# Kernel optimization log

Measured on AMD Instinct MI355X. Metric: run time of the kernel, lower is better.

Reference implementation:

```python
import jax, jax.numpy as jnp
import numpy as np

B, F, V, E, T, NTOK, G, D = 8192, 64, 1000, 64, 2, 16, 4, 256
LN_EPS = 1e-5


def setup_inputs() -> dict:
    key = jax.random.key(0)
    ks = jax.random.split(key, 5)
    int_feats = jax.random.randint(ks[0], (B, F), 0, V, dtype=jnp.int64)
    missing_mask = jax.random.randint(ks[1], (B, F), 0, 2, dtype=jnp.int32)
    # deterministic seeded permutation of features split into NTOK equal groups
    perm = np.random.default_rng(1234).permutation(F)
    group_idx = jnp.asarray(perm.reshape(NTOK, G), dtype=jnp.int32)
    emb_tables = jax.random.normal(ks[2], (T, F, V, E), jnp.float32) * 0.02
    missing_emb = jax.random.normal(ks[3], (T, F, E), jnp.float32) * 0.02
    kW, kb = jax.random.split(ks[4])
    W = jax.random.normal(kW, (D, E * T), jnp.float32) * (1.0 / np.sqrt(E * T))
    b = jnp.zeros((D,), jnp.float32)
    ln_gamma = jnp.ones((D,), jnp.float32)
    ln_beta = jnp.zeros((D,), jnp.float32)
    return {"int_feats": int_feats, "missing_mask": missing_mask,
            "group_idx": group_idx, "emb_tables": emb_tables,
            "missing_emb": missing_emb, "W": W, "b": b,
            "ln_gamma": ln_gamma, "ln_beta": ln_beta}


def reference(int_feats, missing_mask, group_idx, emb_tables, missing_emb, W, b, ln_gamma, ln_beta):
    f_idx = jnp.arange(F)[None, :]  # (1, F) broadcast with (B, F) ids
    # per-table feature embedding gather: [T, B, F, E]
    feats = jax.vmap(lambda tbl: tbl[f_idx, int_feats])(emb_tables)
    # additive missing embeddings
    mask = missing_mask.astype(feats.dtype)
    feats = feats + mask[None, :, :, None] * missing_emb[:, None, :, :]
    # token-group mean pooling: [T, B, NTOK, G, E] -> [T, B, NTOK, E]
    pooled = feats[:, :, group_idx, :].mean(axis=3)
    # concat tables along feature dim (table order preserved): [B, NTOK, T*E]
    x = jnp.moveaxis(pooled, 0, 2).reshape(B, NTOK, T * E)
    # Linear -> SiLU -> LayerNorm
    h = jax.nn.silu(x @ W.T + b)
    mu = h.mean(-1, keepdims=True)
    var = ((h - mu) ** 2).mean(-1, keepdims=True)
    return (h - mu) * jax.lax.rsqrt(var + LN_EPS) * ln_gamma + ln_beta
```

## Files before the change

### kernel.cpp

```cpp
#include <hip/hip_runtime.h>
#include <math.h>

#define B_    8192
#define F_    64
#define V_    1000
#define E_    64
#define T_    2
#define NTOK_ 16
#define G_    4
#define D_    256
#define K_    128
#define LN_EPS 1e-5f

#define RPB   2
#define TOK2  (NTOK_ * RPB)
#define XSP   136
#define HSP   260

typedef __attribute__((ext_vector_type(8))) short  frag_ab;
typedef __attribute__((ext_vector_type(4))) float  frag_cd;
typedef __attribute__((ext_vector_type(4))) float  f32x4;

static __device__ __forceinline__ unsigned short f2bf(float f) {
    unsigned int u = __float_as_uint(f);
    u += 0x7FFFu + ((u >> 16) & 1u);
    return (unsigned short)(u >> 16);
}

__global__ __launch_bounds__(256) void convert_w_kernel(const float* __restrict__ W,
                                                        unsigned int* __restrict__ Wb_packed) {
    const int i = blockIdx.x * 256 + threadIdx.x;
    if (i < (D_ * K_) / 2) {
        const float2 v = *(const float2*)(W + (size_t)i * 2);
        const unsigned int p = (unsigned int)f2bf(v.x) | ((unsigned int)f2bf(v.y) << 16);
        __builtin_nontemporal_store(p, Wb_packed + i);
    }
}

__global__ __launch_bounds__(256, 4) void fused_tokenizer_kernel(
    const int*   __restrict__ int_feats,
    const int*   __restrict__ missing_mask,
    const int*   __restrict__ group_idx,
    const float* __restrict__ emb_tables,
    const float* __restrict__ missing_emb,
    const unsigned short* __restrict__ Wb,
    const float* __restrict__ bias,
    const float* __restrict__ gamma,
    const float* __restrict__ beta,
    float*       __restrict__ out)
{
    __shared__ __align__(16) char smem[TOK2 * HSP * 4];
    unsigned short (*xs)[XSP] = (unsigned short (*)[XSP])smem;
    float          (*hs)[HSP] = (float (*)[HSP])smem;

    __shared__ int   sid[RPB][F_];
    __shared__ int   smask[RPB][F_];
    __shared__ int   sg[NTOK_ * G_];
    __shared__ float ps [TOK2][4];
    __shared__ float pss[TOK2][4];

    const int tid  = threadIdx.x;
    const int b0   = blockIdx.x * RPB;
    const int lane = tid & 63;
    const int wave = tid >> 6;

    if (tid < RPB * F_) {
        const int r = tid >> 6, f = tid & 63;
        sid[r][f]   = int_feats[(b0 + r) * F_ + f];
        smask[r][f] = missing_mask[(b0 + r) * F_ + f];
    }
    if (tid < F_) sg[tid] = group_idx[tid];
    __syncthreads();

#pragma unroll
    for (int i = 0; i < 4; ++i) {
        const int c   = i * 256 + tid;
        const int row = c >> 9;
        const int cc  = c & 511;
        const int n   = cc >> 5;
        const int r4  = cc & 31;
        const int t   = r4 >> 4;
        const int e   = (r4 & 15) * 4;

        float4 ev[G_], mv[G_];
        float  mk[G_];
#pragma unroll
        for (int g = 0; g < G_; ++g) {
            const int f  = sg[n * G_ + g];
            const int id = sid[row][f];
            ev[g] = *(const float4*)(emb_tables + (((size_t)(t * F_ + f) * V_) + id) * E_ + e);
            mv[g] = *(const float4*)(missing_emb + (size_t)(t * F_ + f) * E_ + e);
            mk[g] = (float)smask[row][f];
        }
        float ax = 0.f, ay = 0.f, az = 0.f, aw = 0.f;
#pragma unroll
        for (int g = 0; g < G_; ++g) {
            ax += ev[g].x + mk[g] * mv[g].x;
            ay += ev[g].y + mk[g] * mv[g].y;
            az += ev[g].z + mk[g] * mv[g].z;
            aw += ev[g].w + mk[g] * mv[g].w;
        }
        union { unsigned int u[2]; } pk;
        pk.u[0] = (unsigned int)f2bf(0.25f * ax) | ((unsigned int)f2bf(0.25f * ay) << 16);
        pk.u[1] = (unsigned int)f2bf(0.25f * az) | ((unsigned int)f2bf(0.25f * aw) << 16);
        *(uint2*)(&xs[row * NTOK_ + n][r4 * 4]) = make_uint2(pk.u[0], pk.u[1]);
    }
    __syncthreads();

    const int m = lane & 15;
    const int q = lane >> 4;

    frag_ab a0[4], a1[4];
#pragma unroll
    for (int s = 0; s < 4; ++s) {
        a0[s] = *(const frag_ab*)(&xs[m][32 * s + 8 * q]);
        a1[s] = *(const frag_ab*)(&xs[NTOK_ + m][32 * s + 8 * q]);
    }
    __syncthreads();

    float s0 = 0.f, ss0 = 0.f, s1 = 0.f, ss1 = 0.f;

    frag_ab wb_[2][4];
    {
        const unsigned short* wp = Wb + (size_t)((wave * 4 + 0) * 16 + m) * K_ + 8 * q;
#pragma unroll
        for (int s = 0; s < 4; ++s) wb_[0][s] = *(const frag_ab*)(wp + 32 * s);
    }

#pragma unroll
    for (int tt = 0; tt < 4; ++tt) {
        const int cur = tt & 1;
        if (tt < 3) {
            const unsigned short* wp = Wb + (size_t)((wave * 4 + tt + 1) * 16 + m) * K_ + 8 * q;
#pragma unroll
            for (int s = 0; s < 4; ++s) wb_[cur ^ 1][s] = *(const frag_ab*)(wp + 32 * s);
        }
        frag_cd acc0 = {0.f, 0.f, 0.f, 0.f};
        frag_cd acc1 = {0.f, 0.f, 0.f, 0.f};
#pragma unroll
        for (int s = 0; s < 4; ++s) {
            acc0 = __builtin_amdgcn_mfma_f32_16x16x32_bf16(wb_[cur][s], a0[s], acc0, 0, 0, 0);
            acc1 = __builtin_amdgcn_mfma_f32_16x16x32_bf16(wb_[cur][s], a1[s], acc1, 0, 0, 0);
        }
        const int nt  = wave * 4 + tt;
        const int col = nt * 16 + q * 4;
        const float4 bn = *(const float4*)(bias + col);
        const float bnv[4] = {bn.x, bn.y, bn.z, bn.w};
        float4 h0, h1;
#pragma unroll
        for (int reg = 0; reg < 4; ++reg) {
            const float z0 = acc0[reg] + bnv[reg];
            const float z1 = acc1[reg] + bnv[reg];
            const float v0 = z0 / (1.f + __expf(-z0));
            const float v1 = z1 / (1.f + __expf(-z1));
            s0 += v0; ss0 += v0 * v0;
            s1 += v1; ss1 += v1 * v1;
            ((float*)&h0)[reg] = v0;
            ((float*)&h1)[reg] = v1;
        }
        *(float4*)(&hs[m][col])         = h0;
        *(float4*)(&hs[NTOK_ + m][col]) = h1;
    }

    s0  += __shfl_xor(s0,  16, 64);  ss0 += __shfl_xor(ss0, 16, 64);
    s0  += __shfl_xor(s0,  32, 64);  ss0 += __shfl_xor(ss0, 32, 64);
    s1  += __shfl_xor(s1,  16, 64);  ss1 += __shfl_xor(ss1, 16, 64);
    s1  += __shfl_xor(s1,  32, 64);  ss1 += __shfl_xor(ss1, 32, 64);
    if (q == 0) {
        ps [m][wave] = s0;  pss[m][wave] = ss0;
        ps [NTOK_ + m][wave] = s1;  pss[NTOK_ + m][wave] = ss1;
    }
    __syncthreads();

    const float4 gm = *(const float4*)(gamma + lane * 4);
    const float4 bt = *(const float4*)(beta  + lane * 4);
#pragma unroll
    for (int qq = 0; qq < 8; ++qq) {
        const int n = wave * 8 + qq;
        const float4 p4  = *(const float4*)(&ps[n][0]);
        const float4 pq4 = *(const float4*)(&pss[n][0]);
        const float s_tot  = (p4.x  + p4.y)  + (p4.z  + p4.w);
        const float ss_tot = (pq4.x + pq4.y) + (pq4.z + pq4.w);
        const float mu   = s_tot * (1.f / D_);
        const float var  = ss_tot * (1.f / D_) - mu * mu;
        const float rsig = rsqrtf(var + LN_EPS);

        const float4 v = *(const float4*)(&hs[n][lane * 4]);
        f32x4 o;
        o.x = (v.x - mu) * rsig * gm.x + bt.x;
        o.y = (v.y - mu) * rsig * gm.y + bt.y;
        o.z = (v.z - mu) * rsig * gm.z + bt.z;
        o.w = (v.w - mu) * rsig * gm.w + bt.w;
        const size_t orow = ((size_t)(b0 + (n >> 4)) * NTOK_ + (n & 15)) * D_;
        __builtin_nontemporal_store(o, (f32x4*)(out + orow + lane * 4));
    }
}

extern "C" void kernel_launch(void* const* d_in, const int* in_sizes, int n_in,
                              void* d_out, int out_size, void* d_ws, size_t ws_size,
                              hipStream_t stream) {
    const int*   int_feats    = (const int*)  d_in[0];
    const int*   missing_mask = (const int*)  d_in[1];
    const int*   group_idx    = (const int*)  d_in[2];
    const float* emb_tables   = (const float*)d_in[3];
    const float* missing_emb  = (const float*)d_in[4];
    const float* W            = (const float*)d_in[5];
    const float* bias         = (const float*)d_in[6];
    const float* gamma        = (const float*)d_in[7];
    const float* beta         = (const float*)d_in[8];
    float* out = (float*)d_out;

    unsigned short* Wb = (unsigned short*)d_ws;

    convert_w_kernel<<<(D_ * K_ / 2 + 255) / 256, 256, 0, stream>>>(W, (unsigned int*)Wb);
    fused_tokenizer_kernel<<<B_ / RPB, 256, 0, stream>>>(
        int_feats, missing_mask, group_idx, emb_tables, missing_emb,
        Wb, bias, gamma, beta, out);
}
```

Measured before the change: 222.9 us.

## Halve LDS staging buffer and precompute gather byte offsets for higher occupancy

The shared h staging buffer now holds only one row's 16 tokens. The second row's SiLU outputs are kept in registers and written back after the first row's LayerNorm has been stored, with an extra barrier between the two passes. The gather prologue now precomputes per-(row, table, token, group) byte offsets and mask values in shared memory, which removes the dependent index lookups inside the gather loop. The occupancy hint rises from 4 to 6 blocks per CU. In exchange the kernel gains extra barriers and register pressure, and the larger occupancy target may force register spills.

```diff
diff --git a/kernel.cpp b/kernel.cpp
--- a/kernel.cpp
+++ b/kernel.cpp
@@ -37,7 +37,7 @@
     }
 }
 
-__global__ __launch_bounds__(256, 4) void fused_tokenizer_kernel(
+__global__ __launch_bounds__(256, 6) void fused_tokenizer_kernel(
     const int*   __restrict__ int_feats,
     const int*   __restrict__ missing_mask,
     const int*   __restrict__ group_idx,
@@ -49,13 +49,13 @@
     const float* __restrict__ beta,
     float*       __restrict__ out)
 {
-    __shared__ __align__(16) char smem[TOK2 * HSP * 4];
+    __shared__ __align__(16) char smem[NTOK_ * HSP * 4];
     unsigned short (*xs)[XSP] = (unsigned short (*)[XSP])smem;
     float          (*hs)[HSP] = (float (*)[HSP])smem;
 
-    __shared__ int   sid[RPB][F_];
-    __shared__ int   smask[RPB][F_];
-    __shared__ int   sg[NTOK_ * G_];
+    __shared__ unsigned int poff[RPB][T_][NTOK_][G_];
+    __shared__ unsigned int moff[T_][NTOK_][G_];
+    __shared__ float        pmk [RPB][NTOK_][G_];
     __shared__ float ps [TOK2][4];
     __shared__ float pss[TOK2][4];
 
@@ -64,14 +64,21 @@
     const int lane = tid & 63;
     const int wave = tid >> 6;
 
-    if (tid < RPB * F_) {
-        const int r = tid >> 6, f = tid & 63;
-        sid[r][f]   = int_feats[(b0 + r) * F_ + f];
-        smask[r][f] = missing_mask[(b0 + r) * F_ + f];
-    }
-    if (tid < F_) sg[tid] = group_idx[tid];
-    __syncthreads();
-
+    {
+        const int row = tid >> 7;
+        const int t   = (tid >> 6) & 1;
+        const int n   = (tid >> 2) & 15;
+        const int g   = tid & 3;
+        const int f   = group_idx[n * G_ + g];
+        const int id  = int_feats[(b0 + row) * F_ + f];
+        poff[row][t][n][g] = (unsigned int)(((t * F_ + f) * V_ + id) * (E_ * 4));
+        if (row == 0) moff[t][n][g] = (unsigned int)((t * F_ + f) * (E_ * 4));
+        if (t == 0)   pmk[row][n][g] = (float)missing_mask[(b0 + row) * F_ + f];
+    }
+    __syncthreads();
+
+    const char* tbl = (const char*)emb_tables;
+    const char* msb = (const char*)missing_emb;
 #pragma unroll
     for (int i = 0; i < 4; ++i) {
         const int c   = i * 256 + tid;
@@ -80,17 +87,15 @@
         const int n   = cc >> 5;
         const int r4  = cc & 31;
         const int t   = r4 >> 4;
-        const int e   = (r4 & 15) * 4;
+        const int eb  = (r4 & 15) * 16;
 
         float4 ev[G_], mv[G_];
         float  mk[G_];
 #pragma unroll
         for (int g = 0; g < G_; ++g) {
-            const int f  = sg[n * G_ + g];
-            const int id = sid[row][f];
-            ev[g] = *(const float4*)(emb_tables + (((size_t)(t * F_ + f) * V_) + id) * E_ + e);
-            mv[g] = *(const float4*)(missing_emb + (size_t)(t * F_ + f) * E_ + e);
-            mk[g] = (float)smask[row][f];
+            ev[g] = *(const float4*)(tbl + poff[row][t][n][g] + eb);
+            mv[g] = *(const float4*)(msb + moff[t][n][g] + eb);
+            mk[g] = pmk[row][n][g];
         }
         float ax = 0.f, ay = 0.f, az = 0.f, aw = 0.f;
 #pragma unroll
@@ -119,6 +124,7 @@
     __syncthreads();
 
     float s0 = 0.f, ss0 = 0.f, s1 = 0.f, ss1 = 0.f;
+    float4 h1r[4];
 
     frag_ab wb_[2][4];
     {
@@ -142,11 +148,10 @@
             acc0 = __builtin_amdgcn_mfma_f32_16x16x32_bf16(wb_[cur][s], a0[s], acc0, 0, 0, 0);
             acc1 = __builtin_amdgcn_mfma_f32_16x16x32_bf16(wb_[cur][s], a1[s], acc1, 0, 0, 0);
         }
-        const int nt  = wave * 4 + tt;
-        const int col = nt * 16 + q * 4;
+        const int col = (wave * 4 + tt) * 16 + q * 4;
         const float4 bn = *(const float4*)(bias + col);
         const float bnv[4] = {bn.x, bn.y, bn.z, bn.w};
-        float4 h0, h1;
+        float4 h0;
 #pragma unroll
         for (int reg = 0; reg < 4; ++reg) {
             const float z0 = acc0[reg] + bnv[reg];
@@ -155,11 +160,10 @@
             const float v1 = z1 / (1.f + __expf(-z1));
             s0 += v0; ss0 += v0 * v0;
             s1 += v1; ss1 += v1 * v1;
-            ((float*)&h0)[reg] = v0;
-            ((float*)&h1)[reg] = v1;
-        }
-        *(float4*)(&hs[m][col])         = h0;
-        *(float4*)(&hs[NTOK_ + m][col]) = h1;
+            ((float*)&h0)[reg]      = v0;
+            ((float*)&h1r[tt])[reg] = v1;
+        }
+        *(float4*)(&hs[m][col]) = h0;
     }
 
     s0  += __shfl_xor(s0,  16, 64);  ss0 += __shfl_xor(ss0, 16, 64);
@@ -167,7 +171,7 @@
     s1  += __shfl_xor(s1,  16, 64);  ss1 += __shfl_xor(ss1, 16, 64);
     s1  += __shfl_xor(s1,  32, 64);  ss1 += __shfl_xor(ss1, 32, 64);
     if (q == 0) {
-        ps [m][wave] = s0;  pss[m][wave] = ss0;
+        ps [m][wave]         = s0;  pss[m][wave]         = ss0;
         ps [NTOK_ + m][wave] = s1;  pss[NTOK_ + m][wave] = ss1;
     }
     __syncthreads();
@@ -175,8 +179,8 @@
     const float4 gm = *(const float4*)(gamma + lane * 4);
     const float4 bt = *(const float4*)(beta  + lane * 4);
 #pragma unroll
-    for (int qq = 0; qq < 8; ++qq) {
-        const int n = wave * 8 + qq;
+    for (int qq = 0; qq < 4; ++qq) {
+        const int n = wave * 4 + qq;
         const float4 p4  = *(const float4*)(&ps[n][0]);
         const float4 pq4 = *(const float4*)(&pss[n][0]);
         const float s_tot  = (p4.x  + p4.y)  + (p4.z  + p4.w);
@@ -191,8 +195,35 @@
         o.y = (v.y - mu) * rsig * gm.y + bt.y;
         o.z = (v.z - mu) * rsig * gm.z + bt.z;
         o.w = (v.w - mu) * rsig * gm.w + bt.w;
-        const size_t orow = ((size_t)(b0 + (n >> 4)) * NTOK_ + (n & 15)) * D_;
-        __builtin_nontemporal_store(o, (f32x4*)(out + orow + lane * 4));
+        __builtin_nontemporal_store(o, (f32x4*)(out + ((size_t)b0 * NTOK_ + n) * D_ + lane * 4));
+    }
+    __syncthreads();
+
+#pragma unroll
+    for (int tt = 0; tt < 4; ++tt) {
+        const int col = (wave * 4 + tt) * 16 + q * 4;
+        *(float4*)(&hs[m][col]) = h1r[tt];
+    }
+    __syncthreads();
+
+#pragma unroll
+    for (int qq = 0; qq < 4; ++qq) {
+        const int n = wave * 4 + qq;
+        const float4 p4  = *(const float4*)(&ps[NTOK_ + n][0]);
+        const float4 pq4 = *(const float4*)(&pss[NTOK_ + n][0]);
+        const float s_tot  = (p4.x  + p4.y)  + (p4.z  + p4.w);
+        const float ss_tot = (pq4.x + pq4.y) + (pq4.z + pq4.w);
+        const float mu   = s_tot * (1.f / D_);
+        const float var  = ss_tot * (1.f / D_) - mu * mu;
+        const float rsig = rsqrtf(var + LN_EPS);
+
+        const float4 v = *(const float4*)(&hs[n][lane * 4]);
+        f32x4 o;
+        o.x = (v.x - mu) * rsig * gm.x + bt.x;
+        o.y = (v.y - mu) * rsig * gm.y + bt.y;
+        o.z = (v.z - mu) * rsig * gm.z + bt.z;
+        o.w = (v.w - mu) * rsig * gm.w + bt.w;
+        __builtin_nontemporal_store(o, (f32x4*)(out + ((size_t)(b0 + 1) * NTOK_ + n) * D_ + lane * 4));
     }
 }
 
```

Result: no change. 227.1 us (+1.9%).

## Convert embedding tables to fp16 each call to halve gather traffic

Applied to the files above, without the earlier changes.

Adds a conversion kernel that writes fp16 copies of the embedding tables and missing embeddings into the workspace every call. The fused kernel then gathers 8-wide fp16 vectors instead of fp32 float4s, halving the bytes moved per gathered row and reducing the cache footprint of the random gathers. The price is a full pass over the 32 MB fp32 table (read plus fp16 write) on every call, and a small precision loss before the bf16 rounding. The old fp32 kernel is kept as a fallback when the workspace is too small.

```diff
diff --git a/kernel.cpp b/kernel.cpp
--- a/kernel.cpp
+++ b/kernel.cpp
@@ -17,9 +17,10 @@
 #define XSP   136
 #define HSP   260
 
-typedef __attribute__((ext_vector_type(8))) short  frag_ab;
-typedef __attribute__((ext_vector_type(4))) float  frag_cd;
-typedef __attribute__((ext_vector_type(4))) float  f32x4;
+typedef __attribute__((ext_vector_type(8))) short    frag_ab;
+typedef __attribute__((ext_vector_type(4))) float    frag_cd;
+typedef __attribute__((ext_vector_type(4))) float    f32x4;
+typedef __attribute__((ext_vector_type(8))) _Float16 h8;
 
 static __device__ __forceinline__ unsigned short f2bf(float f) {
     unsigned int u = __float_as_uint(f);
@@ -37,7 +38,177 @@
     }
 }
 
+__global__ __launch_bounds__(256) void convert_f16_kernel(const float* __restrict__ src,
+                                                          _Float16* __restrict__ dst, int n8) {
+    const int i = blockIdx.x * 256 + threadIdx.x;
+    if (i < n8) {
+        const float4 a = *(const float4*)(src + (size_t)i * 8);
+        const float4 b = *(const float4*)(src + (size_t)i * 8 + 4);
+        h8 o;
+        o[0] = (_Float16)a.x; o[1] = (_Float16)a.y; o[2] = (_Float16)a.z; o[3] = (_Float16)a.w;
+        o[4] = (_Float16)b.x; o[5] = (_Float16)b.y; o[6] = (_Float16)b.z; o[7] = (_Float16)b.w;
+        *(h8*)(dst + (size_t)i * 8) = o;
+    }
+}
+
 __global__ __launch_bounds__(256, 4) void fused_tokenizer_kernel(
+    const int*   __restrict__ int_feats,
+    const int*   __restrict__ missing_mask,
+    const int*   __restrict__ group_idx,
+    const _Float16* __restrict__ tblh,
+    const _Float16* __restrict__ mish,
+    const unsigned short* __restrict__ Wb,
+    const float* __restrict__ bias,
+    const float* __restrict__ gamma,
+    const float* __restrict__ beta,
+    float*       __restrict__ out)
+{
+    __shared__ __align__(16) char smem[TOK2 * HSP * 4];
+    unsigned short (*xs)[XSP] = (unsigned short (*)[XSP])smem;
+    float          (*hs)[HSP] = (float (*)[HSP])smem;
+
+    __shared__ int   sid[RPB][F_];
+    __shared__ int   smask[RPB][F_];
+    __shared__ int   sg[NTOK_ * G_];
+    __shared__ float ps [TOK2][4];
+    __shared__ float pss[TOK2][4];
+
+    const int tid  = threadIdx.x;
+    const int b0   = blockIdx.x * RPB;
+    const int lane = tid & 63;
+    const int wave = tid >> 6;
+
+    if (tid < RPB * F_) {
+        const int r = tid >> 6, f = tid & 63;
+        sid[r][f]   = int_feats[(b0 + r) * F_ + f];
+        smask[r][f] = missing_mask[(b0 + r) * F_ + f];
+    }
+    if (tid < F_) sg[tid] = group_idx[tid];
+    __syncthreads();
+
+#pragma unroll
+    for (int i = 0; i < 2; ++i) {
+        const int c   = i * 256 + tid;
+        const int row = c >> 8;
+        const int n   = (c >> 4) & 15;
+        const int t   = (c >> 3) & 1;
+        const int e8  = c & 7;
+
+        h8    ev[G_], mv[G_];
+        float mk[G_];
+#pragma unroll
+        for (int g = 0; g < G_; ++g) {
+            const int f  = sg[n * G_ + g];
+            const int id = sid[row][f];
+            ev[g] = *(const h8*)(tblh + ((size_t)((t * F_ + f) * V_) + id) * E_ + e8 * 8);
+            mv[g] = *(const h8*)(mish + (size_t)(t * F_ + f) * E_ + e8 * 8);
+            mk[g] = (float)smask[row][f];
+        }
+        float acc[8] = {0.f, 0.f, 0.f, 0.f, 0.f, 0.f, 0.f, 0.f};
+#pragma unroll
+        for (int g = 0; g < G_; ++g)
+#pragma unroll
+            for (int j = 0; j < 8; ++j)
+                acc[j] += (float)ev[g][j] + mk[g] * (float)mv[g][j];
+        unsigned int pk[4];
+#pragma unroll
+        for (int jj = 0; jj < 4; ++jj)
+            pk[jj] = (unsigned int)f2bf(0.25f * acc[2 * jj])
+                   | ((unsigned int)f2bf(0.25f * acc[2 * jj + 1]) << 16);
+        *(uint4*)(&xs[row * NTOK_ + n][(t * 8 + e8) * 8]) = make_uint4(pk[0], pk[1], pk[2], pk[3]);
+    }
+    __syncthreads();
+
+    const int m = lane & 15;
+    const int q = lane >> 4;
+
+    frag_ab a0[4], a1[4];
+#pragma unroll
+    for (int s = 0; s < 4; ++s) {
+        a0[s] = *(const frag_ab*)(&xs[m][32 * s + 8 * q]);
+        a1[s] = *(const frag_ab*)(&xs[NTOK_ + m][32 * s + 8 * q]);
+    }
+    __syncthreads();
+
+    float s0 = 0.f, ss0 = 0.f, s1 = 0.f, ss1 = 0.f;
+
+    frag_ab wb_[2][4];
+    {
+        const unsigned short* wp = Wb + (size_t)((wave * 4 + 0) * 16 + m) * K_ + 8 * q;
+#pragma unroll
+        for (int s = 0; s < 4; ++s) wb_[0][s] = *(const frag_ab*)(wp + 32 * s);
+    }
+
+#pragma unroll
+    for (int tt = 0; tt < 4; ++tt) {
+        const int cur = tt & 1;
+        if (tt < 3) {
+            const unsigned short* wp = Wb + (size_t)((wave * 4 + tt + 1) * 16 + m) * K_ + 8 * q;
+#pragma unroll
+            for (int s = 0; s < 4; ++s) wb_[cur ^ 1][s] = *(const frag_ab*)(wp + 32 * s);
+        }
+        frag_cd acc0 = {0.f, 0.f, 0.f, 0.f};
+        frag_cd acc1 = {0.f, 0.f, 0.f, 0.f};
+#pragma unroll
+        for (int s = 0; s < 4; ++s) {
+            acc0 = __builtin_amdgcn_mfma_f32_16x16x32_bf16(wb_[cur][s], a0[s], acc0, 0, 0, 0);
+            acc1 = __builtin_amdgcn_mfma_f32_16x16x32_bf16(wb_[cur][s], a1[s], acc1, 0, 0, 0);
+        }
+        const int nt  = wave * 4 + tt;
+        const int col = nt * 16 + q * 4;
+        const float4 bn = *(const float4*)(bias + col);
+        const float bnv[4] = {bn.x, bn.y, bn.z, bn.w};
+        float4 h0, h1;
+#pragma unroll
+        for (int reg = 0; reg < 4; ++reg) {
+            const float z0 = acc0[reg] + bnv[reg];
+            const float z1 = acc1[reg] + bnv[reg];
+            const float v0 = z0 / (1.f + __expf(-z0));
+            const float v1 = z1 / (1.f + __expf(-z1));
+            s0 += v0; ss0 += v0 * v0;
+            s1 += v1; ss1 += v1 * v1;
+            ((float*)&h0)[reg] = v0;
+            ((float*)&h1)[reg] = v1;
+        }
+        *(float4*)(&hs[m][col])         = h0;
+        *(float4*)(&hs[NTOK_ + m][col]) = h1;
+    }
+
+    s0  += __shfl_xor(s0,  16, 64);  ss0 += __shfl_xor(ss0, 16, 64);
+    s0  += __shfl_xor(s0,  32, 64);  ss0 += __shfl_xor(ss0, 32, 64);
+    s1  += __shfl_xor(s1,  16, 64);  ss1 += __shfl_xor(ss1, 16, 64);
+    s1  += __shfl_xor(s1,  32, 64);  ss1 += __shfl_xor(ss1, 32, 64);
+    if (q == 0) {
+        ps [m][wave]         = s0;  pss[m][wave]         = ss0;
+        ps [NTOK_ + m][wave] = s1;  pss[NTOK_ + m][wave] = ss1;
+    }
+    __syncthreads();
+
+    const float4 gm = *(const float4*)(gamma + lane * 4);
+    const float4 bt = *(const float4*)(beta  + lane * 4);
+#pragma unroll
+    for (int qq = 0; qq < 8; ++qq) {
+        const int n = wave * 8 + qq;
+        const float4 p4  = *(const float4*)(&ps[n][0]);
+        const float4 pq4 = *(const float4*)(&pss[n][0]);
+        const float s_tot  = (p4.x  + p4.y)  + (p4.z  + p4.w);
+        const float ss_tot = (pq4.x + pq4.y) + (pq4.z + pq4.w);
+        const float mu   = s_tot * (1.f / D_);
+        const float var  = ss_tot * (1.f / D_) - mu * mu;
+        const float rsig = rsqrtf(var + LN_EPS);
+
+        const float4 v = *(const float4*)(&hs[n][lane * 4]);
+        f32x4 o;
+        o.x = (v.x - mu) * rsig * gm.x + bt.x;
+        o.y = (v.y - mu) * rsig * gm.y + bt.y;
+        o.z = (v.z - mu) * rsig * gm.z + bt.z;
+        o.w = (v.w - mu) * rsig * gm.w + bt.w;
+        const size_t orow = ((size_t)(b0 + (n >> 4)) * NTOK_ + (n & 15)) * D_;
+        __builtin_nontemporal_store(o, (f32x4*)(out + orow + lane * 4));
+    }
+}
+
+__global__ __launch_bounds__(256, 4) void fused_tokenizer_fp32_kernel(
     const int*   __restrict__ int_feats,
     const int*   __restrict__ missing_mask,
     const int*   __restrict__ group_idx,
@@ -167,7 +338,7 @@
     s1  += __shfl_xor(s1,  16, 64);  ss1 += __shfl_xor(ss1, 16, 64);
     s1  += __shfl_xor(s1,  32, 64);  ss1 += __shfl_xor(ss1, 32, 64);
     if (q == 0) {
-        ps [m][wave] = s0;  pss[m][wave] = ss0;
+        ps [m][wave]         = s0;  pss[m][wave]         = ss0;
         ps [NTOK_ + m][wave] = s1;  pss[NTOK_ + m][wave] = ss1;
     }
     __syncthreads();
@@ -211,9 +382,25 @@
     float* out = (float*)d_out;
 
     unsigned short* Wb = (unsigned short*)d_ws;
+    const size_t wb_bytes  = (size_t)D_ * K_ * 2;
+    const size_t tbl_bytes = (size_t)T_ * F_ * V_ * E_ * 2;
+    const size_t mis_bytes = (size_t)T_ * F_ * E_ * 2;
+    _Float16* tblh = (_Float16*)((char*)d_ws + wb_bytes);
+    _Float16* mish = (_Float16*)((char*)d_ws + wb_bytes + tbl_bytes);
 
     convert_w_kernel<<<(D_ * K_ / 2 + 255) / 256, 256, 0, stream>>>(W, (unsigned int*)Wb);
-    fused_tokenizer_kernel<<<B_ / RPB, 256, 0, stream>>>(
-        int_feats, missing_mask, group_idx, emb_tables, missing_emb,
-        Wb, bias, gamma, beta, out);
-}
+
+    if (ws_size >= wb_bytes + tbl_bytes + mis_bytes) {
+        const int n8_tbl = T_ * F_ * V_ * E_ / 8;
+        const int n8_mis = T_ * F_ * E_ / 8;
+        convert_f16_kernel<<<(n8_tbl + 255) / 256, 256, 0, stream>>>(emb_tables, tblh, n8_tbl);
+        convert_f16_kernel<<<(n8_mis + 255) / 256, 256, 0, stream>>>(missing_emb, mish, n8_mis);
+        fused_tokenizer_kernel<<<B_ / RPB, 256, 0, stream>>>(
+            int_feats, missing_mask, group_idx, tblh, mish,
+            Wb, bias, gamma, beta, out);
+    } else {
+        fused_tokenizer_fp32_kernel<<<B_ / RPB, 256, 0, stream>>>(
+            int_feats, missing_mask, group_idx, emb_tables, missing_emb,
+            Wb, bias, gamma, beta, out);
+    }
+}
```

After: 221.6 us. No clear change (-0.6%).
